# Optimization experiments

Measured on AMD Instinct MI355X. Metric: run time of the kernel, lower is better.

Reference implementation:

```python
import jax, jax.numpy as jnp
import numpy as np

B, S, D, H = 2, 2048, 1024, 16
HD = D // H


def setup_inputs() -> dict:
    key = jax.random.key(0)
    ks = jax.random.split(key, 5)
    scale = 0.02
    x = jax.random.normal(ks[0], (B, S, D), dtype=jnp.float32)
    Wq = jax.random.normal(ks[1], (D, D), dtype=jnp.float32) * scale
    Wk = jax.random.normal(ks[2], (D, D), dtype=jnp.float32) * scale
    Wv = jax.random.normal(ks[3], (D, D), dtype=jnp.float32) * scale
    Wo = jax.random.normal(ks[4], (D, D), dtype=jnp.float32) * scale
    z = jnp.zeros((D,), dtype=jnp.float32)
    return {"x": x, "Wq": Wq, "bq": z, "Wk": Wk, "bk": z, "Wv": Wv, "bv": z, "Wo": Wo, "bo": z}


def reference(x, Wq, bq, Wk, bk, Wv, bv, Wo, bo):
    b, s, d = x.shape
    hd = d // H
    # QKV projections -> [b, H, s, hd]
    def heads(W, bias):
        return (x @ W.T + bias).reshape(b, s, H, hd).transpose(0, 2, 1, 3)
    q = heads(Wq, bq)
    k = heads(Wk, bk)
    v = heads(Wv, bv)
    scale = 1.0 / np.sqrt(hd).astype(np.float32)
    attn = scale * jnp.einsum('bhqd,bhkd->bhqk', q, k)  # [b,H,s,s]
    # causal mask (attn dropout p=0 is identity before masking)
    causal = jnp.tril(jnp.ones((s, s), dtype=bool))
    attn = jnp.where(causal[None, None], attn, -jnp.inf)
    attn = jax.nn.softmax(attn, axis=-1)
    ans = jnp.einsum('bhqk,bhkd->bhqd', attn, v)
    ans = ans.transpose(0, 2, 1, 3).reshape(b, s, d)
    return ans @ Wo.T + bo
```

## Files before the change

kernel.cpp:

```cpp
#include <hip/hip_runtime.h>

#define DEV __device__ __forceinline__

typedef __attribute__((ext_vector_type(8))) __bf16 bf16x8;
typedef __attribute__((ext_vector_type(4))) float f32x4;
typedef __attribute__((ext_vector_type(16))) float f32x16;
typedef __attribute__((ext_vector_type(4))) unsigned short u16x4;
typedef __attribute__((ext_vector_type(8))) unsigned short u16x8;
typedef __attribute__((ext_vector_type(2))) unsigned u32x2;

DEV unsigned short f2bf(float f) {
  unsigned u = __builtin_bit_cast(unsigned, f);
  u += 0x7FFFu + ((u >> 16) & 1u);
  return (unsigned short)(u >> 16);
}

DEV f32x4 mfma16(bf16x8 a, bf16x8 b, f32x4 c) {
  return __builtin_amdgcn_mfma_f32_16x16x32_bf16(a, b, c, 0, 0, 0);
}
DEV f32x16 mfma32(bf16x8 a, bf16x8 b, f32x16 c) {
  return __builtin_amdgcn_mfma_f32_32x32x16_bf16(a, b, c, 0, 0, 0);
}

DEV void gload16(const void* g, void* l) {
  __builtin_amdgcn_global_load_lds(
      (const __attribute__((address_space(1))) unsigned int*)g,
      (__attribute__((address_space(3))) unsigned int*)l, 16, 0, 0);
}

DEV void plswap(unsigned& x, unsigned& y) {
#if __has_builtin(__builtin_amdgcn_permlane32_swap)
  u32x2 r = __builtin_amdgcn_permlane32_swap(x, y, false, false);
  x = r[0];
  y = r[1];
#else
  unsigned sx = __shfl_xor(x, 32, 64), sy = __shfl_xor(y, 32, 64);
  int hi = (threadIdx.x & 63) >> 5;
  unsigned nx = hi ? sy : x;
  unsigned ny = hi ? y : sx;
  x = nx;
  y = ny;
#endif
}
DEV float xadd32(float v) {
  unsigned a = __builtin_bit_cast(unsigned, v), b = a;
  plswap(a, b);
  return __builtin_bit_cast(float, a) + __builtin_bit_cast(float, b);
}

__global__ __launch_bounds__(256) void k_cvt_all(
    const float* __restrict__ x,
    const float* __restrict__ Wq, const float* __restrict__ Wk,
    const float* __restrict__ Wv, const float* __restrict__ Wo,
    unsigned short* __restrict__ xb,
    unsigned short* __restrict__ Wqb, unsigned short* __restrict__ Wkb,
    unsigned short* __restrict__ Wvb, unsigned short* __restrict__ Wob) {
  int g = blockIdx.x * 256 + threadIdx.x;
  const float* src;
  unsigned short* dst;
  int loc;
  if (g < 524288) {
    src = x; dst = xb; loc = g;
  } else {
    int r = g - 524288;
    int w = r >> 17;
    loc = r & 131071;
    src = w == 0 ? Wq : w == 1 ? Wk : w == 2 ? Wv : Wo;
    dst = w == 0 ? Wqb : w == 1 ? Wkb : w == 2 ? Wvb : Wob;
  }
  int row = loc >> 7, k8 = loc & 127;
  const f32x4* s = (const f32x4*)(src + ((size_t)row << 10) + (k8 << 3));
  f32x4 a = s[0], b = s[1];
  u16x8 o;
  o[0] = f2bf(a[0]); o[1] = f2bf(a[1]); o[2] = f2bf(a[2]); o[3] = f2bf(a[3]);
  o[4] = f2bf(b[0]); o[5] = f2bf(b[1]); o[6] = f2bf(b[2]); o[7] = f2bf(b[3]);
  *(u16x8*)(dst + ((size_t)row << 10) + ((k8 << 3) ^ ((row & 7) << 3))) = o;
}

DEV void gemm_mainloop(const char* Ag, const char* Bg, char* lds,
                       int lane, int wid, f32x4 acc[4][4]) {
  int g4 = lane >> 4, r16 = lane & 15;
  int wm = wid >> 1, wn = wid & 1;
  int adA[2], adB[2];
#pragma unroll
  for (int ks = 0; ks < 2; ++ks) {
    int swz = ((ks * 4 + g4) ^ (lane & 7)) << 4;
    adA[ks] = (wm * 64 + r16) * 128 + swz;
    adB[ks] = 16384 + (wn * 64 + r16) * 128 + swz;
  }
  int o0 = wid * 4096 + lane * 16;
  int grow[4], ginr[4];
#pragma unroll
  for (int i = 0; i < 4; ++i) {
    grow[i] = (o0 + i * 1024) >> 7;
    ginr[i] = (o0 + i * 1024) & 127;
  }
  auto STAGE = [&](int KT, int BASE) {
#pragma unroll
    for (int i = 0; i < 4; ++i) {
      int oo = o0 + i * 1024;
      size_t gofs = (size_t)grow[i] * 2048 + (size_t)KT * 128 + ginr[i];
      gload16(Ag + gofs, lds + BASE + oo);
      gload16(Bg + gofs, lds + BASE + 16384 + oo);
    }
  };
  STAGE(0, 0);
  for (int kt = 0; kt < 16; ++kt) {
    int cur = (kt & 1) << 15;
    if (kt + 1 < 16) {
      STAGE(kt + 1, cur ^ 32768);
      asm volatile("s_waitcnt vmcnt(8)" ::: "memory");
    } else {
      asm volatile("s_waitcnt vmcnt(0)" ::: "memory");
    }
    __builtin_amdgcn_s_barrier();
    __builtin_amdgcn_sched_barrier(0);
#pragma unroll
    for (int ks = 0; ks < 2; ++ks) {
      bf16x8 af[4], bfr[4];
#pragma unroll
      for (int i = 0; i < 4; ++i) {
        af[i]  = *(const bf16x8*)(lds + cur + adA[ks] + i * 2048);
        bfr[i] = *(const bf16x8*)(lds + cur + adB[ks] + i * 2048);
      }
      __builtin_amdgcn_s_setprio(1);
#pragma unroll
      for (int mi = 0; mi < 4; ++mi)
#pragma unroll
        for (int ni = 0; ni < 4; ++ni)
          acc[mi][ni] = mfma16(af[mi], bfr[ni], acc[mi][ni]);
      __builtin_amdgcn_s_setprio(0);
    }
    asm volatile("s_waitcnt lgkmcnt(0)" ::: "memory");
    __builtin_amdgcn_sched_barrier(0);
    __builtin_amdgcn_s_barrier();
  }
}

__global__ __launch_bounds__(256) void k_gemm_qkv(
    const unsigned short* __restrict__ xb,
    const unsigned short* __restrict__ Wqb, const unsigned short* __restrict__ Wkb,
    const unsigned short* __restrict__ Wvb,
    const float* __restrict__ bq, const float* __restrict__ bk,
    const float* __restrict__ bv,
    unsigned short* __restrict__ Qb, unsigned short* __restrict__ Kb,
    unsigned short* __restrict__ Vt) {
  __shared__ char lds[65536];
  int tid = threadIdx.x, lane = tid & 63, wid = tid >> 6;
  int bm = blockIdx.x & 31, bn = blockIdx.x >> 5;
  int r0 = bm * 128;
  int colT = bn * 128;
  int which = colT >> 10;
  int ncol = colT & 1023;
  const unsigned short* Wb = which == 0 ? Wqb : which == 1 ? Wkb : Wvb;
  f32x4 acc[4][4] = {};
  gemm_mainloop((const char*)xb + (size_t)r0 * 2048,
                (const char*)Wb + (size_t)ncol * 2048, lds, lane, wid, acc);
  int g4 = lane >> 4, r16 = lane & 15, wm = wid >> 1, wn = wid & 1;
  const float* bias = which == 0 ? bq : which == 1 ? bk : bv;
  float oscale = which == 0 ? 0.18033688f : 1.0f;
  int ncolw = ncol + wn * 64;
#pragma unroll
  for (int ni = 0; ni < 4; ++ni) {
    int gcol = ncolw + ni * 16 + r16;
    float bvv = bias[gcol];
    int h = gcol >> 6, hd = gcol & 63;
#pragma unroll
    for (int mi = 0; mi < 4; ++mi) {
      int growb = r0 + wm * 64 + mi * 16 + g4 * 4;
      int bb = growb >> 11, s0 = growb & 2047;
      if (which == 2) {
        u16x4 pk;
#pragma unroll
        for (int jj = 0; jj < 4; ++jj) pk[jj] = f2bf(acc[mi][ni][jj] + bvv);
        *(u16x4*)(Vt + ((size_t)(bb * 16 + h) * 64 + hd) * 2048 + s0) = pk;
      } else {
        unsigned short* dst = which == 0 ? Qb : Kb;
        size_t base = ((size_t)(bb * 16 + h) * 2048 + s0) * 64 + hd;
#pragma unroll
        for (int jj = 0; jj < 4; ++jj)
          dst[base + (size_t)jj * 64] = f2bf((acc[mi][ni][jj] + bvv) * oscale);
      }
    }
  }
}

__global__ __launch_bounds__(128) void k_attn(
    const unsigned short* __restrict__ Q, const unsigned short* __restrict__ K,
    const unsigned short* __restrict__ Vt, unsigned short* __restrict__ ansb,
    float* __restrict__ PO, float* __restrict__ PL) {
  __shared__ char lds[2 * 16384];
#define SG(c, a, bb2, jj) \
  ((unsigned)(c) | ((unsigned)(a) << 8) | ((unsigned)(bb2) << 16) | ((unsigned)(jj) << 24))
  static const unsigned SEGT[80] = {
    SG(31,0,8,0),  SG(31,8,16,1), SG(31,16,24,2), SG(31,24,32,3),
    SG(30,7,15,1), SG(30,15,23,2), SG(30,23,31,3),
    SG(29,7,15,1), SG(29,22,30,3), SG(28,21,29,3),
    SG(23,0,8,0),  SG(23,8,16,1), SG(23,16,24,2),
    SG(22,7,15,1), SG(22,15,23,2), SG(21,14,22,2),
    SG(15,0,8,0),  SG(15,8,16,1), SG(14,7,15,1),  SG(7,0,8,0),
    SG(30,0,7,0),  SG(29,0,7,0),  SG(29,15,22,2),
    SG(28,0,7,0),  SG(28,7,14,1), SG(28,14,21,2),
    SG(27,0,7,0),  SG(27,7,14,1), SG(27,14,21,2), SG(27,21,28,3),
    SG(26,6,13,1), SG(26,13,20,2), SG(26,20,27,3),
    SG(25,6,13,1), SG(25,19,26,3), SG(24,18,25,3),
    SG(22,0,7,0),  SG(21,0,7,0),  SG(21,7,14,1),
    SG(20,0,7,0),  SG(20,7,14,1), SG(20,14,21,2),
    SG(19,6,13,1), SG(19,13,20,2), SG(18,12,19,2),
    SG(14,0,7,0),  SG(13,0,7,0),  SG(13,7,14,1),
    SG(12,6,13,1), SG(6,0,7,0),
    SG(26,0,6,0),  SG(25,0,6,0),  SG(25,13,19,2),
    SG(24,0,6,0),  SG(24,6,12,1), SG(24,12,18,2),
    SG(19,0,6,0),  SG(18,0,6,0),  SG(18,6,12,1),
    SG(17,0,6,0),  SG(17,6,12,1), SG(17,12,18,2),
    SG(16,5,11,1), SG(16,11,17,2),
    SG(12,0,6,0),  SG(11,0,6,0),  SG(11,6,12,1),
    SG(10,5,11,1), SG(5,0,6,0),
    SG(16,0,5,0), SG(10,0,5,0), SG(9,0,5,0), SG(9,5,10,1), SG(8,4,9,1),
    SG(4,0,5,0),
    SG(8,0,4,0), SG(3,0,4,0), SG(2,0,3,0), SG(1,0,2,0), SG(0,0,1,0)
  };
#undef SG
  int tid = threadIdx.x, lane = tid & 63, wid = tid >> 6;
  int l31 = lane & 31, hi = lane >> 5;
  int bid = blockIdx.x;
  int bh = (bid & 7) * 4 + ((bid >> 3) & 3);
  unsigned se = SEGT[bid >> 5];
  int c = se & 255, t0 = (se >> 8) & 255, t1 = (se >> 16) & 255, j = se >> 24;
  bool direct = (c < 8);
  int pidx = (bh * 24 + (c - 8)) * 4 + j;
  int b = bh >> 4, h = bh & 15;
  int q0 = c * 64 + wid * 32;
  const unsigned short* Qh = Q + (size_t)bh * (2048 * 64);
  const char* Kg = (const char*)(K + (size_t)bh * (2048 * 64));
  const char* Vg = (const char*)(Vt + (size_t)bh * (64 * 2048));

  int kof[4], ko[4], vo[4];
#pragma unroll
  for (int i = 0; i < 4; ++i) {
    int o = tid * 16 + i * 2048;
    int row = o >> 7, cc = o & 127;
    int sc = cc ^ ((row & 7) << 4);
    kof[i] = o;
    ko[i] = row * 128 + sc;
    vo[i] = row * 4096 + sc;
  }

  bf16x8 qf[4];
#pragma unroll
  for (int ks = 0; ks < 4; ++ks)
    qf[ks] = *(const bf16x8*)(Qh + (size_t)(q0 + l31) * 64 + ks * 16 + hi * 8);

  f32x16 O0 = {}, O1 = {}, l16 = {};
  int swzl = (l31 & 7) << 4;
  int hioff = hi * 16;

  auto STAGEA = [&](int T, int BASE) {
    size_t kK = (size_t)T * 8192;
    size_t kV = (size_t)T * 128;
#pragma unroll
    for (int i = 0; i < 4; ++i) {
      gload16(Kg + kK + ko[i], lds + BASE + kof[i]);
      gload16(Vg + kV + vo[i], lds + BASE + 8192 + kof[i]);
    }
  };

  STAGEA(t0, 0);
  for (int t = t0; t < t1; ++t) {
    int cur = ((t - t0) & 1) << 14;
    if (t + 1 < t1) {
      STAGEA(t + 1, cur ^ 16384);
      asm volatile("s_waitcnt vmcnt(8)" ::: "memory");
    } else {
      asm volatile("s_waitcnt vmcnt(0)" ::: "memory");
    }
    __builtin_amdgcn_s_barrier();
    __builtin_amdgcn_sched_barrier(0);
    const char* KL = lds + cur;
    const char* VL = KL + 8192;
    f32x16 s0 = {}, s1 = {};
    __builtin_amdgcn_s_setprio(1);
#pragma unroll
    for (int ks = 0; ks < 4; ++ks) {
      bf16x8 kf0 = *(const bf16x8*)(KL + l31 * 128 + ((ks * 32 + hioff) ^ swzl));
      bf16x8 kf1 = *(const bf16x8*)(KL + (32 + l31) * 128 + ((ks * 32 + hioff) ^ swzl));
      s0 = mfma32(kf0, qf[ks], s0);
      s1 = mfma32(kf1, qf[ks], s1);
    }
    __builtin_amdgcn_s_setprio(0);
    if (t == c) {
      int lim2 = q0 + l31 - t * 64 - 4 * hi;
#pragma unroll
      for (int r = 0; r < 16; ++r) {
        int kc = (r & 3) + 8 * (r >> 2);
        if (kc > lim2) s0[r] = -1e30f;
        if (kc + 32 > lim2) s1[r] = -1e30f;
      }
    }
#pragma unroll
    for (int r = 0; r < 16; ++r) {
      s0[r] = __builtin_amdgcn_exp2f(s0[r]);
      s1[r] = __builtin_amdgcn_exp2f(s1[r]);
      l16[r] += s0[r] + s1[r];
    }
    __builtin_amdgcn_s_setprio(1);
#define PV_CHUNK(SV, E, C16) { \
    unsigned x0, x1, y0, y1; \
    asm("v_cvt_pk_bf16_f32 %0, %1, %2" : "=v"(x0) : "v"(SV[8*(E)+0]), "v"(SV[8*(E)+1])); \
    asm("v_cvt_pk_bf16_f32 %0, %1, %2" : "=v"(x1) : "v"(SV[8*(E)+2]), "v"(SV[8*(E)+3])); \
    asm("v_cvt_pk_bf16_f32 %0, %1, %2" : "=v"(y0) : "v"(SV[8*(E)+4]), "v"(SV[8*(E)+5])); \
    asm("v_cvt_pk_bf16_f32 %0, %1, %2" : "=v"(y1) : "v"(SV[8*(E)+6]), "v"(SV[8*(E)+7])); \
    plswap(x0, y0); \
    plswap(x1, y1); \
    union { unsigned u[4]; bf16x8 v; } pf; \
    pf.u[0] = x0; \
    pf.u[1] = x1; \
    pf.u[2] = y0; \
    pf.u[3] = y1; \
    bf16x8 v0 = *(const bf16x8*)(VL + l31 * 128 + (((C16) * 32 + hioff) ^ swzl)); \
    bf16x8 v1 = *(const bf16x8*)(VL + (32 + l31) * 128 + (((C16) * 32 + hioff) ^ swzl)); \
    O0 = mfma32(pf.v, v0, O0); \
    O1 = mfma32(pf.v, v1, O1); }
    PV_CHUNK(s0, 0, 0)
    PV_CHUNK(s0, 1, 1)
    PV_CHUNK(s1, 0, 2)
    PV_CHUNK(s1, 1, 3)
#undef PV_CHUNK
    __builtin_amdgcn_s_setprio(0);
    asm volatile("s_waitcnt lgkmcnt(0)" ::: "memory");
    __builtin_amdgcn_sched_barrier(0);
    __builtin_amdgcn_s_barrier();
  }
  float a[16];
#pragma unroll
  for (int r = 0; r < 16; ++r) a[r] = l16[r];
#pragma unroll
  for (int st2 = 8; st2 >= 1; st2 >>= 1)
#pragma unroll
    for (int i = 0; i < st2; ++i) a[i] += a[i + st2];
  float lf = xadd32(a[0]);
  __syncthreads();
  char* wb = lds + wid * 128;
  if (direct) {
    float rl = 1.f / lf;
    if (lane < 32) *(float*)(wb + l31 * 4) = rl;
    asm volatile("s_waitcnt lgkmcnt(0)" ::: "memory");
    f32x4 rv0 = *(const f32x4*)(wb + hioff);
    f32x4 rv1 = *(const f32x4*)(wb + 32 + hioff);
    f32x4 rv2 = *(const f32x4*)(wb + 64 + hioff);
    f32x4 rv3 = *(const f32x4*)(wb + 96 + hioff);
#pragma unroll
    for (int r = 0; r < 16; ++r) {
      float sc = (r < 4 ? rv0 : r < 8 ? rv1 : r < 12 ? rv2 : rv3)[r & 3];
      int rowl = q0 + (r & 3) + 8 * (r >> 2) + 4 * hi;
      int rowg = (b << 11) + rowl;
      int cswz = (rowl & 7) << 3;
      int cg0 = (h << 6) + l31;
      int cg1 = (h << 6) + 32 + l31;
      ansb[(size_t)rowg * 1024 + (cg0 ^ cswz)] = f2bf(O0[r] * sc);
      ansb[(size_t)rowg * 1024 + (cg1 ^ cswz)] = f2bf(O1[r] * sc);
    }
  } else {
    float* po = PO + (size_t)pidx * 4096;
#pragma unroll
    for (int r = 0; r < 16; ++r) {
      int rowl = wid * 32 + (r & 3) + 8 * (r >> 2) + 4 * hi;
      po[rowl * 64 + l31] = O0[r];
      po[rowl * 64 + 32 + l31] = O1[r];
    }
    if (hi == 0) PL[pidx * 64 + wid * 32 + l31] = lf;
  }
}

__global__ __launch_bounds__(256) void k_attn_combine(
    const float* __restrict__ PO, const float* __restrict__ PL,
    unsigned short* __restrict__ ansb) {
  int bid = blockIdx.x;
  int bh = bid & 31, cc = 8 + (bid >> 5);
  int nseg = cc < 16 ? 2 : cc < 24 ? 3 : 4;
  int b = bh >> 4, h = bh & 15;
  int t = threadIdx.x;
  int r = t >> 2, c4 = (t & 3) << 4;
  int pbase = (bh * 24 + (cc - 8)) * 4;
  f32x4 s0 = {}, s1 = {}, s2 = {}, s3 = {};
  float lsum = 0.f;
  for (int j = 0; j < nseg; ++j) {
    const float* A = PO + (size_t)(pbase + j) * 4096 + r * 64 + c4;
    s0 += *(const f32x4*)(A + 0);
    s1 += *(const f32x4*)(A + 4);
    s2 += *(const f32x4*)(A + 8);
    s3 += *(const f32x4*)(A + 12);
    lsum += PL[(pbase + j) * 64 + r];
  }
  float rl = 1.f / lsum;
  u16x8 o0, o1;
#pragma unroll
  for (int j = 0; j < 4; ++j) {
    o0[j] = f2bf(s0[j] * rl);
    o0[4 + j] = f2bf(s1[j] * rl);
    o1[j] = f2bf(s2[j] * rl);
    o1[4 + j] = f2bf(s3[j] * rl);
  }
  int rowg = (b << 11) + cc * 64 + r;
  int colg = (h << 6) + c4;
  int cswz = (rowg & 7) << 3;
  *(u16x8*)(ansb + (size_t)rowg * 1024 + (colg ^ cswz)) = o0;
  *(u16x8*)(ansb + (size_t)rowg * 1024 + ((colg + 8) ^ cswz)) = o1;
}

__global__ __launch_bounds__(256) void k_gemm_out(
    const unsigned short* __restrict__ ansb, const unsigned short* __restrict__ Wob,
    const float* __restrict__ bo, float* __restrict__ out) {
  __shared__ char lds[65536];
  int tid = threadIdx.x, lane = tid & 63, wid = tid >> 6;
  int bm = blockIdx.x & 31, bn = blockIdx.x >> 5;
  int r0 = bm * 128, c0 = bn * 128;
  f32x4 acc[4][4] = {};
  gemm_mainloop((const char*)ansb + (size_t)r0 * 2048,
                (const char*)Wob + (size_t)c0 * 2048, lds, lane, wid, acc);
  int g4 = lane >> 4, r16 = lane & 15, wm = wid >> 1, wn = wid & 1;
#pragma unroll
  for (int ni = 0; ni < 4; ++ni) {
    int gcol = c0 + wn * 64 + ni * 16 + r16;
    float bvv = bo[gcol];
#pragma unroll
    for (int mi = 0; mi < 4; ++mi) {
      int growb = r0 + wm * 64 + mi * 16 + g4 * 4;
#pragma unroll
      for (int jj = 0; jj < 4; ++jj)
        out[(size_t)(growb + jj) * 1024 + gcol] = acc[mi][ni][jj] + bvv;
    }
  }
}

extern "C" void kernel_launch(void* const* d_in, const int* in_sizes, int n_in,
                              void* d_out, int out_size, void* d_ws, size_t ws_size,
                              hipStream_t stream) {
  const float* x  = (const float*)d_in[0];
  const float* Wq = (const float*)d_in[1];
  const float* bq = (const float*)d_in[2];
  const float* Wk = (const float*)d_in[3];
  const float* bk = (const float*)d_in[4];
  const float* Wv = (const float*)d_in[5];
  const float* bv = (const float*)d_in[6];
  const float* Wo = (const float*)d_in[7];
  const float* bo = (const float*)d_in[8];
  char* ws = (char*)d_ws;
  unsigned short* xb   = (unsigned short*)(ws);
  unsigned short* ansb = (unsigned short*)(ws);
  unsigned short* Wqb  = (unsigned short*)(ws + (8u  << 20));
  unsigned short* Wkb  = (unsigned short*)(ws + (10u << 20));
  unsigned short* Wvb  = (unsigned short*)(ws + (12u << 20));
  unsigned short* Wob  = (unsigned short*)(ws + (14u << 20));
  unsigned short* Qb   = (unsigned short*)(ws + (16u << 20));
  unsigned short* Kb   = (unsigned short*)(ws + (24u << 20));
  unsigned short* Vt   = (unsigned short*)(ws + (32u << 20));
  float*          PO   = (float*)(ws + (40u << 20));
  float*          PL   = (float*)(ws + (88u << 20));

  k_cvt_all<<<4096, 256, 0, stream>>>(x, Wq, Wk, Wv, Wo, xb, Wqb, Wkb, Wvb, Wob);
  k_gemm_qkv<<<768, 256, 0, stream>>>(xb, Wqb, Wkb, Wvb, bq, bk, bv, Qb, Kb, Vt);
  k_attn<<<2560, 128, 0, stream>>>(Qb, Kb, Vt, ansb, PO, PL);
  k_attn_combine<<<768, 256, 0, stream>>>(PO, PL, ansb);
  k_gemm_out<<<256, 256, 0, stream>>>(ansb, Wob, bo, (float*)d_out);
}
```

Measured before the change: 104.8 us.

## Double query tile per attention block to reuse staged K/V tiles

Each attention workgroup now processes 128 query rows (two 32-row groups per wave) instead of 64, so every K/V tile staged into LDS feeds twice the MFMA work. The split-KV segment table is rebuilt for 16 query chunks, the grid is halved, and the partial-output/combine indexing is updated to match. This is meant to cut global K/V traffic and per-block overhead, at the cost of more registers per wave and fewer blocks for load balancing across CUs.

Measured after the change: 119.1 us. 13.6% more time.

```diff
diff --git a/kernel.cpp b/kernel.cpp
--- a/kernel.cpp
+++ b/kernel.cpp
@@ -192,33 +192,20 @@
   __shared__ char lds[2 * 16384];
 #define SG(c, a, bb2, jj) \
   ((unsigned)(c) | ((unsigned)(a) << 8) | ((unsigned)(bb2) << 16) | ((unsigned)(jj) << 24))
-  static const unsigned SEGT[80] = {
-    SG(31,0,8,0),  SG(31,8,16,1), SG(31,16,24,2), SG(31,24,32,3),
-    SG(30,7,15,1), SG(30,15,23,2), SG(30,23,31,3),
-    SG(29,7,15,1), SG(29,22,30,3), SG(28,21,29,3),
-    SG(23,0,8,0),  SG(23,8,16,1), SG(23,16,24,2),
-    SG(22,7,15,1), SG(22,15,23,2), SG(21,14,22,2),
-    SG(15,0,8,0),  SG(15,8,16,1), SG(14,7,15,1),  SG(7,0,8,0),
-    SG(30,0,7,0),  SG(29,0,7,0),  SG(29,15,22,2),
-    SG(28,0,7,0),  SG(28,7,14,1), SG(28,14,21,2),
-    SG(27,0,7,0),  SG(27,7,14,1), SG(27,14,21,2), SG(27,21,28,3),
-    SG(26,6,13,1), SG(26,13,20,2), SG(26,20,27,3),
-    SG(25,6,13,1), SG(25,19,26,3), SG(24,18,25,3),
-    SG(22,0,7,0),  SG(21,0,7,0),  SG(21,7,14,1),
-    SG(20,0,7,0),  SG(20,7,14,1), SG(20,14,21,2),
-    SG(19,6,13,1), SG(19,13,20,2), SG(18,12,19,2),
-    SG(14,0,7,0),  SG(13,0,7,0),  SG(13,7,14,1),
-    SG(12,6,13,1), SG(6,0,7,0),
-    SG(26,0,6,0),  SG(25,0,6,0),  SG(25,13,19,2),
-    SG(24,0,6,0),  SG(24,6,12,1), SG(24,12,18,2),
-    SG(19,0,6,0),  SG(18,0,6,0),  SG(18,6,12,1),
-    SG(17,0,6,0),  SG(17,6,12,1), SG(17,12,18,2),
-    SG(16,5,11,1), SG(16,11,17,2),
-    SG(12,0,6,0),  SG(11,0,6,0),  SG(11,6,12,1),
-    SG(10,5,11,1), SG(5,0,6,0),
-    SG(16,0,5,0), SG(10,0,5,0), SG(9,0,5,0), SG(9,5,10,1), SG(8,4,9,1),
-    SG(4,0,5,0),
-    SG(8,0,4,0), SG(3,0,4,0), SG(2,0,3,0), SG(1,0,2,0), SG(0,0,1,0)
+  static const unsigned SEGT[40] = {
+    SG(3,0,8,0),  SG(7,0,8,0),  SG(7,8,16,1),  SG(10,14,22,2),
+    SG(11,0,8,0), SG(11,8,16,1), SG(11,16,24,2),
+    SG(14,7,15,1), SG(14,22,30,3),
+    SG(15,0,8,0), SG(15,8,16,1), SG(15,16,24,2), SG(15,24,32,3),
+    SG(6,0,7,0),  SG(6,7,14,1),  SG(9,6,13,1),  SG(9,13,20,2),
+    SG(10,0,7,0), SG(10,7,14,1), SG(12,6,13,1), SG(12,19,26,3),
+    SG(13,0,7,0), SG(13,7,14,1), SG(13,14,21,2), SG(13,21,28,3),
+    SG(14,0,7,0), SG(14,15,22,2),
+    SG(2,0,6,0),  SG(5,0,6,0),  SG(5,6,12,1),
+    SG(8,0,6,0),  SG(8,6,12,1), SG(8,12,18,2),
+    SG(9,0,6,0),  SG(12,0,6,0), SG(12,13,19,2),
+    SG(4,0,5,0),  SG(4,5,10,1),
+    SG(1,0,4,0),  SG(0,0,2,0)
   };
 #undef SG
   int tid = threadIdx.x, lane = tid & 63, wid = tid >> 6;
@@ -227,10 +214,10 @@
   int bh = (bid & 7) * 4 + ((bid >> 3) & 3);
   unsigned se = SEGT[bid >> 5];
   int c = se & 255, t0 = (se >> 8) & 255, t1 = (se >> 16) & 255, j = se >> 24;
-  bool direct = (c < 8);
-  int pidx = (bh * 24 + (c - 8)) * 4 + j;
+  bool direct = (c < 4);
+  int pidx = (bh * 12 + (c - 4)) * 4 + j;
   int b = bh >> 4, h = bh & 15;
-  int q0 = c * 64 + wid * 32;
+  int q0 = c * 128 + wid * 64;
   const unsigned short* Qh = Q + (size_t)bh * (2048 * 64);
   const char* Kg = (const char*)(K + (size_t)bh * (2048 * 64));
   const char* Vg = (const char*)(Vt + (size_t)bh * (64 * 2048));
@@ -246,12 +233,16 @@
     vo[i] = row * 4096 + sc;
   }
 
-  bf16x8 qf[4];
-#pragma unroll
-  for (int ks = 0; ks < 4; ++ks)
-    qf[ks] = *(const bf16x8*)(Qh + (size_t)(q0 + l31) * 64 + ks * 16 + hi * 8);
-
-  f32x16 O0 = {}, O1 = {}, l16 = {};
+  bf16x8 qf[2][4];
+#pragma unroll
+  for (int qg = 0; qg < 2; ++qg)
+#pragma unroll
+    for (int ks = 0; ks < 4; ++ks)
+      qf[qg][ks] = *(const bf16x8*)(Qh + (size_t)(q0 + qg * 32 + l31) * 64 +
+                                    ks * 16 + hi * 8);
+
+  f32x16 O[2][2] = {};
+  f32x16 lac[2] = {};
   int swzl = (l31 & 7) << 4;
   int hioff = hi * 16;
 
@@ -278,97 +269,112 @@
     __builtin_amdgcn_sched_barrier(0);
     const char* KL = lds + cur;
     const char* VL = KL + 8192;
-    f32x16 s0 = {}, s1 = {};
-    __builtin_amdgcn_s_setprio(1);
-#pragma unroll
-    for (int ks = 0; ks < 4; ++ks) {
-      bf16x8 kf0 = *(const bf16x8*)(KL + l31 * 128 + ((ks * 32 + hioff) ^ swzl));
-      bf16x8 kf1 = *(const bf16x8*)(KL + (32 + l31) * 128 + ((ks * 32 + hioff) ^ swzl));
-      s0 = mfma32(kf0, qf[ks], s0);
-      s1 = mfma32(kf1, qf[ks], s1);
-    }
-    __builtin_amdgcn_s_setprio(0);
-    if (t == c) {
-      int lim2 = q0 + l31 - t * 64 - 4 * hi;
+#pragma unroll
+    for (int qg = 0; qg < 2; ++qg) {
+      f32x16 s0 = {}, s1 = {};
+      __builtin_amdgcn_s_setprio(1);
+#pragma unroll
+      for (int ks = 0; ks < 4; ++ks) {
+        bf16x8 kf0 = *(const bf16x8*)(KL + l31 * 128 + ((ks * 32 + hioff) ^ swzl));
+        bf16x8 kf1 = *(const bf16x8*)(KL + (32 + l31) * 128 + ((ks * 32 + hioff) ^ swzl));
+        s0 = mfma32(kf0, qf[qg][ks], s0);
+        s1 = mfma32(kf1, qf[qg][ks], s1);
+      }
+      __builtin_amdgcn_s_setprio(0);
+      int qgb = q0 + qg * 32;
+      if (t * 64 + 63 > qgb) {
+        int lim2 = qgb + l31 - t * 64 - 4 * hi;
+#pragma unroll
+        for (int r = 0; r < 16; ++r) {
+          int kc = (r & 3) + 8 * (r >> 2);
+          if (kc > lim2) s0[r] = -1e30f;
+          if (kc + 32 > lim2) s1[r] = -1e30f;
+        }
+      }
 #pragma unroll
       for (int r = 0; r < 16; ++r) {
-        int kc = (r & 3) + 8 * (r >> 2);
-        if (kc > lim2) s0[r] = -1e30f;
-        if (kc + 32 > lim2) s1[r] = -1e30f;
-      }
-    }
-#pragma unroll
-    for (int r = 0; r < 16; ++r) {
-      s0[r] = __builtin_amdgcn_exp2f(s0[r]);
-      s1[r] = __builtin_amdgcn_exp2f(s1[r]);
-      l16[r] += s0[r] + s1[r];
-    }
-    __builtin_amdgcn_s_setprio(1);
+        s0[r] = __builtin_amdgcn_exp2f(s0[r]);
+        s1[r] = __builtin_amdgcn_exp2f(s1[r]);
+        lac[qg][r] += s0[r] + s1[r];
+      }
+      __builtin_amdgcn_s_setprio(1);
 #define PV_CHUNK(SV, E, C16) { \
-    unsigned x0, x1, y0, y1; \
-    asm("v_cvt_pk_bf16_f32 %0, %1, %2" : "=v"(x0) : "v"(SV[8*(E)+0]), "v"(SV[8*(E)+1])); \
-    asm("v_cvt_pk_bf16_f32 %0, %1, %2" : "=v"(x1) : "v"(SV[8*(E)+2]), "v"(SV[8*(E)+3])); \
-    asm("v_cvt_pk_bf16_f32 %0, %1, %2" : "=v"(y0) : "v"(SV[8*(E)+4]), "v"(SV[8*(E)+5])); \
-    asm("v_cvt_pk_bf16_f32 %0, %1, %2" : "=v"(y1) : "v"(SV[8*(E)+6]), "v"(SV[8*(E)+7])); \
-    plswap(x0, y0); \
-    plswap(x1, y1); \
-    union { unsigned u[4]; bf16x8 v; } pf; \
-    pf.u[0] = x0; \
-    pf.u[1] = x1; \
-    pf.u[2] = y0; \
-    pf.u[3] = y1; \
-    bf16x8 v0 = *(const bf16x8*)(VL + l31 * 128 + (((C16) * 32 + hioff) ^ swzl)); \
-    bf16x8 v1 = *(const bf16x8*)(VL + (32 + l31) * 128 + (((C16) * 32 + hioff) ^ swzl)); \
-    O0 = mfma32(pf.v, v0, O0); \
-    O1 = mfma32(pf.v, v1, O1); }
-    PV_CHUNK(s0, 0, 0)
-    PV_CHUNK(s0, 1, 1)
-    PV_CHUNK(s1, 0, 2)
-    PV_CHUNK(s1, 1, 3)
+      unsigned x0, x1, y0, y1; \
+      asm("v_cvt_pk_bf16_f32 %0, %1, %2" : "=v"(x0) : "v"(SV[8*(E)+0]), "v"(SV[8*(E)+1])); \
+      asm("v_cvt_pk_bf16_f32 %0, %1, %2" : "=v"(x1) : "v"(SV[8*(E)+2]), "v"(SV[8*(E)+3])); \
+      asm("v_cvt_pk_bf16_f32 %0, %1, %2" : "=v"(y0) : "v"(SV[8*(E)+4]), "v"(SV[8*(E)+5])); \
+      asm("v_cvt_pk_bf16_f32 %0, %1, %2" : "=v"(y1) : "v"(SV[8*(E)+6]), "v"(SV[8*(E)+7])); \
+      plswap(x0, y0); \
+      plswap(x1, y1); \
+      union { unsigned u[4]; bf16x8 v; } pf; \
+      pf.u[0] = x0; \
+      pf.u[1] = x1; \
+      pf.u[2] = y0; \
+      pf.u[3] = y1; \
+      bf16x8 v0 = *(const bf16x8*)(VL + l31 * 128 + (((C16) * 32 + hioff) ^ swzl)); \
+      bf16x8 v1 = *(const bf16x8*)(VL + (32 + l31) * 128 + (((C16) * 32 + hioff) ^ swzl)); \
+      O[qg][0] = mfma32(pf.v, v0, O[qg][0]); \
+      O[qg][1] = mfma32(pf.v, v1, O[qg][1]); }
+      PV_CHUNK(s0, 0, 0)
+      PV_CHUNK(s0, 1, 1)
+      PV_CHUNK(s1, 0, 2)
+      PV_CHUNK(s1, 1, 3)
 #undef PV_CHUNK
-    __builtin_amdgcn_s_setprio(0);
+      __builtin_amdgcn_s_setprio(0);
+    }
     asm volatile("s_waitcnt lgkmcnt(0)" ::: "memory");
     __builtin_amdgcn_sched_barrier(0);
     __builtin_amdgcn_s_barrier();
   }
-  float a[16];
-#pragma unroll
-  for (int r = 0; r < 16; ++r) a[r] = l16[r];
-#pragma unroll
-  for (int st2 = 8; st2 >= 1; st2 >>= 1)
-#pragma unroll
-    for (int i = 0; i < st2; ++i) a[i] += a[i + st2];
-  float lf = xadd32(a[0]);
+  float lf[2];
+#pragma unroll
+  for (int qg = 0; qg < 2; ++qg) {
+    float a[16];
+#pragma unroll
+    for (int r = 0; r < 16; ++r) a[r] = lac[qg][r];
+#pragma unroll
+    for (int st2 = 8; st2 >= 1; st2 >>= 1)
+#pragma unroll
+      for (int i = 0; i < st2; ++i) a[i] += a[i + st2];
+    lf[qg] = xadd32(a[0]);
+  }
   __syncthreads();
-  char* wb = lds + wid * 128;
+  char* wb = lds + wid * 256;
   if (direct) {
-    float rl = 1.f / lf;
-    if (lane < 32) *(float*)(wb + l31 * 4) = rl;
+#pragma unroll
+    for (int qg = 0; qg < 2; ++qg)
+      if (lane < 32) *(float*)(wb + qg * 128 + l31 * 4) = 1.f / lf[qg];
     asm volatile("s_waitcnt lgkmcnt(0)" ::: "memory");
-    f32x4 rv0 = *(const f32x4*)(wb + hioff);
-    f32x4 rv1 = *(const f32x4*)(wb + 32 + hioff);
-    f32x4 rv2 = *(const f32x4*)(wb + 64 + hioff);
-    f32x4 rv3 = *(const f32x4*)(wb + 96 + hioff);
-#pragma unroll
-    for (int r = 0; r < 16; ++r) {
-      float sc = (r < 4 ? rv0 : r < 8 ? rv1 : r < 12 ? rv2 : rv3)[r & 3];
-      int rowl = q0 + (r & 3) + 8 * (r >> 2) + 4 * hi;
-      int rowg = (b << 11) + rowl;
-      int cswz = (rowl & 7) << 3;
-      int cg0 = (h << 6) + l31;
-      int cg1 = (h << 6) + 32 + l31;
-      ansb[(size_t)rowg * 1024 + (cg0 ^ cswz)] = f2bf(O0[r] * sc);
-      ansb[(size_t)rowg * 1024 + (cg1 ^ cswz)] = f2bf(O1[r] * sc);
+#pragma unroll
+    for (int qg = 0; qg < 2; ++qg) {
+      f32x4 rv0 = *(const f32x4*)(wb + qg * 128 + hioff);
+      f32x4 rv1 = *(const f32x4*)(wb + qg * 128 + 32 + hioff);
+      f32x4 rv2 = *(const f32x4*)(wb + qg * 128 + 64 + hioff);
+      f32x4 rv3 = *(const f32x4*)(wb + qg * 128 + 96 + hioff);
+#pragma unroll
+      for (int r = 0; r < 16; ++r) {
+        float sc = (r < 4 ? rv0 : r < 8 ? rv1 : r < 12 ? rv2 : rv3)[r & 3];
+        int rowl = q0 + qg * 32 + (r & 3) + 8 * (r >> 2) + 4 * hi;
+        int rowg = (b << 11) + rowl;
+        int cswz = (rowl & 7) << 3;
+        int cg0 = (h << 6) + l31;
+        int cg1 = (h << 6) + 32 + l31;
+        ansb[(size_t)rowg * 1024 + (cg0 ^ cswz)] = f2bf(O[qg][0][r] * sc);
+        ansb[(size_t)rowg * 1024 + (cg1 ^ cswz)] = f2bf(O[qg][1][r] * sc);
+      }
     }
   } else {
-    float* po = PO + (size_t)pidx * 4096;
-#pragma unroll
-    for (int r = 0; r < 16; ++r) {
-      int rowl = wid * 32 + (r & 3) + 8 * (r >> 2) + 4 * hi;
-      po[rowl * 64 + l31] = O0[r];
-      po[rowl * 64 + 32 + l31] = O1[r];
-    }
-    if (hi == 0) PL[pidx * 64 + wid * 32 + l31] = lf;
+    float* po = PO + (size_t)pidx * 8192;
+#pragma unroll
+    for (int qg = 0; qg < 2; ++qg) {
+#pragma unroll
+      for (int r = 0; r < 16; ++r) {
+        int rowl = wid * 64 + qg * 32 + (r & 3) + 8 * (r >> 2) + 4 * hi;
+        po[rowl * 64 + l31] = O[qg][0][r];
+        po[rowl * 64 + 32 + l31] = O[qg][1][r];
+      }
+      if (hi == 0) PL[pidx * 128 + wid * 64 + qg * 32 + l31] = lf[qg];
+    }
   }
 }
 
@@ -376,21 +382,22 @@
     const float* __restrict__ PO, const float* __restrict__ PL,
     unsigned short* __restrict__ ansb) {
   int bid = blockIdx.x;
-  int bh = bid & 31, cc = 8 + (bid >> 5);
-  int nseg = cc < 16 ? 2 : cc < 24 ? 3 : 4;
+  int bh = bid & 31, rest = bid >> 5;
+  int cc = 4 + (rest >> 1), sub = rest & 1;
+  int nseg = cc < 8 ? 2 : cc < 12 ? 3 : 4;
   int b = bh >> 4, h = bh & 15;
   int t = threadIdx.x;
-  int r = t >> 2, c4 = (t & 3) << 4;
-  int pbase = (bh * 24 + (cc - 8)) * 4;
+  int r = sub * 64 + (t >> 2), c4 = (t & 3) << 4;
+  int pbase = (bh * 12 + (cc - 4)) * 4;
   f32x4 s0 = {}, s1 = {}, s2 = {}, s3 = {};
   float lsum = 0.f;
   for (int j = 0; j < nseg; ++j) {
-    const float* A = PO + (size_t)(pbase + j) * 4096 + r * 64 + c4;
+    const float* A = PO + (size_t)(pbase + j) * 8192 + r * 64 + c4;
     s0 += *(const f32x4*)(A + 0);
     s1 += *(const f32x4*)(A + 4);
     s2 += *(const f32x4*)(A + 8);
     s3 += *(const f32x4*)(A + 12);
-    lsum += PL[(pbase + j) * 64 + r];
+    lsum += PL[(pbase + j) * 128 + r];
   }
   float rl = 1.f / lsum;
   u16x8 o0, o1;
@@ -401,7 +408,7 @@
     o1[j] = f2bf(s2[j] * rl);
     o1[4 + j] = f2bf(s3[j] * rl);
   }
-  int rowg = (b << 11) + cc * 64 + r;
+  int rowg = (b << 11) + cc * 128 + r;
   int colg = (h << 6) + c4;
   int cswz = (rowg & 7) << 3;
   *(u16x8*)(ansb + (size_t)rowg * 1024 + (colg ^ cswz)) = o0;
@@ -460,7 +467,7 @@
 
   k_cvt_all<<<4096, 256, 0, stream>>>(x, Wq, Wk, Wv, Wo, xb, Wqb, Wkb, Wvb, Wob);
   k_gemm_qkv<<<768, 256, 0, stream>>>(xb, Wqb, Wkb, Wvb, bq, bk, bv, Qb, Kb, Vt);
-  k_attn<<<2560, 128, 0, stream>>>(Qb, Kb, Vt, ansb, PO, PL);
+  k_attn<<<1280, 128, 0, stream>>>(Qb, Kb, Vt, ansb, PO, PL);
   k_attn_combine<<<768, 256, 0, stream>>>(PO, PL, ansb);
   k_gemm_out<<<256, 256, 0, stream>>>(ansb, Wob, bo, (float*)d_out);
 }
```
